# Optimization experiments

Measured on AMD Instinct MI355X. Metric: run time of the kernel, lower is better.

## Reference

```python
import jax, jax.numpy as jnp
import numpy as np
import random as pyrandom

NUM_CENTERS = 512
NUM_ITERS = 10
EPS = 1e-16
SEED = 42


def setup_inputs() -> dict:
    key = jax.random.key(0)
    x = jax.random.normal(key, (4, 16384, 256), dtype=jnp.float32)
    return {"x": x}


def _get_dist(x, v):
    # squared Euclidean distances: [B, N, K]
    x2 = jnp.sum(x * x, axis=-1, keepdims=True)            # [B, N, 1]
    xv = jnp.einsum('bnd,bkd->bnk', x, v)                  # [B, N, K]
    v2 = jnp.sum(v * v, axis=-1)[:, None, :]               # [B, 1, K]
    return jax.nn.relu(x2 - 2.0 * xv + v2)


def _update_u(x, v):
    clusters = jnp.argmin(_get_dist(x, v), axis=-1)        # [B, N]
    return jax.nn.one_hot(clusters, NUM_CENTERS, dtype=x.dtype)  # [B, N, K]


def _update_v(x, u):
    # normalize memberships over the points axis (torch dim=1 == axis -2 here)
    un = (u + EPS) / (jnp.sum(u, axis=-2, keepdims=True) + EPS)
    return jnp.einsum('bnk,bnd->bkd', un, x)               # [B, K, d]


def reference(x):
    n = x.shape[-2]
    pyrandom.seed(SEED)
    inds = np.asarray(pyrandom.sample(range(n), NUM_CENTERS))
    # initialization happens under no_grad in the original module
    v0 = jax.lax.stop_gradient(x[..., inds, :])            # [B, K, d]
    u0 = jax.lax.stop_gradient(_update_u(x, v0))

    def step(carry, _):
        _, v = carry
        u_new = _update_u(x, v)
        v_new = _update_v(x, u_new)
        return (u_new, v_new), None

    (u, v), _ = jax.lax.scan(step, (u0, v0), None, length=NUM_ITERS)
    return (u, v)
```

## Files before the change

kernel.cpp:

```cpp
#include <hip/hip_runtime.h>
#include <string.h>

#define B 4
#define N 16384
#define D 256
#define K 512
#define ITERS 10

typedef short short8 __attribute__((ext_vector_type(8)));
typedef float float4v __attribute__((ext_vector_type(4)));

static void host_sample_inds(int* out) {
    static unsigned int mt[624];
    mt[0] = 19650218u;
    for (int i = 1; i < 624; i++)
        mt[i] = 1812433253u * (mt[i - 1] ^ (mt[i - 1] >> 30)) + (unsigned)i;
    {
        int i = 1, j = 0;
        for (int kk = 624; kk; kk--) {
            mt[i] = (mt[i] ^ ((mt[i - 1] ^ (mt[i - 1] >> 30)) * 1664525u)) + 42u + (unsigned)j;
            i++; j++;
            if (i >= 624) { mt[0] = mt[623]; i = 1; }
            if (j >= 1) j = 0;
        }
        for (int kk = 623; kk; kk--) {
            mt[i] = (mt[i] ^ ((mt[i - 1] ^ (mt[i - 1] >> 30)) * 1566083941u)) - (unsigned)i;
            i++;
            if (i >= 624) { mt[0] = mt[623]; i = 1; }
        }
        mt[0] = 0x80000000u;
    }
    static unsigned char seen[N];
    memset(seen, 0, sizeof(seen));
    int mti = 624;
    int got = 0;
    while (got < K) {
        if (mti >= 624) {
            for (int kk = 0; kk < 624; kk++) {
                unsigned int yy = (mt[kk] & 0x80000000u) | (mt[(kk + 1) % 624] & 0x7fffffffu);
                mt[kk] = mt[(kk + 397) % 624] ^ (yy >> 1) ^ ((yy & 1u) ? 0x9908b0dfu : 0u);
            }
            mti = 0;
        }
        unsigned int y = mt[mti++];
        y ^= y >> 11; y ^= (y << 7) & 0x9d2c5680u; y ^= (y << 15) & 0xefc60000u; y ^= y >> 18;
        unsigned int r = y >> 17;
        if (r >= (unsigned)N) continue;
        if (seen[r]) continue;
        seen[r] = 1;
        out[got++] = (int)r;
    }
}

__device__ inline void gload_lds16(const void* g, void* l) {
    __builtin_amdgcn_global_load_lds((const __attribute__((address_space(1))) void*)g,
                                     (__attribute__((address_space(3))) void*)l, 16, 0, 0);
}

__device__ inline unsigned bf16_rne(float f) {
    unsigned u = __float_as_uint(f);
    return (u + 0x7fffu + ((u >> 16) & 1u)) >> 16;
}

__device__ inline unsigned long long shfl_xor_u64(unsigned long long v, int off) {
    int lo = __shfl_xor((int)(unsigned)(v & 0xffffffffull), off);
    int hi = __shfl_xor((int)(unsigned)(v >> 32), off);
    return ((unsigned long long)(unsigned)hi << 32) | (unsigned)lo;
}


__global__ void k_gather_v0(const float* __restrict__ x, const int* __restrict__ inds,
                            float* __restrict__ v) {
    int bk = blockIdx.x; int b = bk / K, k = bk % K;
    int n = inds[k];
    const float4* src = (const float4*)(x + ((size_t)b * N + n) * D);
    float4* dst = (float4*)(v + ((size_t)b * K + k) * D);
    dst[threadIdx.x] = src[threadIdx.x];
}

__global__ void k_totsum(const float* __restrict__ x, float* __restrict__ totsum) {
    int b = blockIdx.y;
    int n0 = blockIdx.x * (N / 64);
    int t = threadIdx.x;
    const float* xb = x + (size_t)b * N * D;
    float s = 0.f;
    for (int n = n0; n < n0 + N / 64; n++) s += xb[(size_t)n * D + t];
    atomicAdd(&totsum[b * D + t], s);
}

__global__ void k_prep(const float* __restrict__ src, unsigned short* __restrict__ cat,
                       float* __restrict__ sq, float* __restrict__ resn,
                       float* __restrict__ lon) {
    int wave = threadIdx.x >> 6, lane = threadIdx.x & 63;
    int row = blockIdx.x * 4 + wave;
    float4 f = ((const float4*)(src + (size_t)row * D))[lane];
    float comp[4] = {f.x, f.y, f.z, f.w};
    unsigned short h[4], l[4];
    float r2 = 0.f, l2 = 0.f, n2 = 0.f;
    #pragma unroll
    for (int j = 0; j < 4; j++) {
        n2 += comp[j] * comp[j];
        unsigned hi = bf16_rne(comp[j]);
        float hif = __uint_as_float(hi << 16);
        float r = comp[j] - hif;
        unsigned lo = bf16_rne(r);
        float lof = __uint_as_float(lo << 16);
        float res = r - lof;
        r2 += res * res;
        l2 += lof * lof;
        h[j] = (unsigned short)hi; l[j] = (unsigned short)lo;
    }
    unsigned short* orow = cat + (size_t)row * 512;
    *(ushort4*)&orow[lane * 4] = make_ushort4(h[0], h[1], h[2], h[3]);
    *(ushort4*)&orow[256 + lane * 4] = make_ushort4(l[0], l[1], l[2], l[3]);
    #pragma unroll
    for (int off = 32; off; off >>= 1) {
        r2 += __shfl_xor(r2, off);
        l2 += __shfl_xor(l2, off);
        n2 += __shfl_xor(n2, off);
    }
    if (lane == 0) { sq[row] = n2; resn[row] = sqrtf(r2); lon[row] = sqrtf(l2); }
}

__global__ void k_errmax(const float* __restrict__ v2, const float* __restrict__ vres,
                         const float* __restrict__ vlo,
                         float* __restrict__ vmaxs, float* __restrict__ vresmaxs,
                         float* __restrict__ vlomaxs) {
    __shared__ float s1[256], s2[256], s3[256];
    int b = blockIdx.x, t = threadIdx.x;
    s1[t] = fmaxf(sqrtf(v2[b * K + t]), sqrtf(v2[b * K + 256 + t]));
    s2[t] = fmaxf(vres[b * K + t], vres[b * K + 256 + t]);
    s3[t] = fmaxf(vlo[b * K + t], vlo[b * K + 256 + t]);
    __syncthreads();
    for (int s = 128; s; s >>= 1) {
        if (t < s) {
            s1[t] = fmaxf(s1[t], s1[t + s]);
            s2[t] = fmaxf(s2[t], s2[t + s]);
            s3[t] = fmaxf(s3[t], s3[t + s]);
        }
        __syncthreads();
    }
    if (t == 0) { vmaxs[b] = s1[0]; vresmaxs[b] = s2[0]; vlomaxs[b] = s3[0]; }
}

__global__ void k_transpose(const float* __restrict__ v, float* __restrict__ vT) {
    int idx = blockIdx.x * 256 + threadIdx.x;
    int d = idx & 255, c = (idx >> 8) & 511, b = idx >> 17;
    vT[((size_t)b * D + d) * K + c] = v[idx];
}

__global__ __launch_bounds__(256, 2) void k_gemm_assign(
    const unsigned short* __restrict__ xcat, const unsigned short* __restrict__ vcat,
    const float* __restrict__ x2, const float* __restrict__ v2,
    const float* __restrict__ xres, const float* __restrict__ xlo,
    const float* __restrict__ vmaxs, const float* __restrict__ vresmaxs,
    const float* __restrict__ vlomaxs,
    int* __restrict__ assign, int* __restrict__ counts,
    int* __restrict__ refine_cnt, int* __restrict__ refine_pt) {
    __shared__ __align__(16) unsigned short As[2][128 * 64];
    __shared__ __align__(16) unsigned short Bs[2][128 * 64];
    __shared__ float x2s[128];
    __shared__ float v2s[512];
    __shared__ unsigned long long candk[128][2][2];
    int b = blockIdx.y;
    int n0 = blockIdx.x * 128;
    int tid = threadIdx.x;
    int wv = tid >> 6, lane = tid & 63;
    int wr = wv >> 1, wc = wv & 1;
    int quad = lane >> 4, l16 = lane & 15;
    const unsigned short* xb = xcat + ((size_t)b * N + n0) * 512;
    const unsigned short* vb0 = vcat + (size_t)b * K * 512;

    if (tid < 128) x2s[tid] = x2[b * N + n0 + tid];
    v2s[tid] = v2[b * K + tid];
    v2s[tid + 256] = v2[b * K + 256 + tid];

    int lds8[4], srow[4], schunk[4];
    #pragma unroll
    for (int i = 0; i < 4; i++) {
        int l = i * 256 + wv * 64 + lane;
        lds8[i] = l * 8;
        srow[i] = l >> 3;
        schunk[i] = ((l & 7) ^ ((l >> 3) & 7)) * 8;
    }

    float4v acc[4][4];
    #pragma unroll
    for (int i = 0; i < 4; i++)
        #pragma unroll
        for (int j = 0; j < 4; j++) acc[i][j] = (float4v){0.f, 0.f, 0.f, 0.f};

    unsigned long long k1[16], k2[16];
    #pragma unroll
    for (int i = 0; i < 16; i++) { k1[i] = ~0ull; k2[i] = ~0ull; }

    #pragma unroll
    for (int i = 0; i < 4; i++) {
        gload_lds16(xb + (size_t)srow[i] * 512 + schunk[i], (void*)&As[0][lds8[i]]);
        gload_lds16(vb0 + (size_t)srow[i] * 512 + schunk[i], (void*)&Bs[0][lds8[i]]);
    }
    __syncthreads();

    for (int ch = 0; ch < 4; ch++) {
        for (int kt = 0; kt < 12; kt++) {
            int cur = kt & 1;
            int nkt = kt + 1, nch = ch;
            if (nkt == 12) { nkt = 0; nch++; }
            if (nch < 4) {
                int k4 = (nkt & 3) * 64;
                int kcolA = (nkt < 8) ? k4 : 256 + k4;
                int kcolB = (nkt < 4) ? k4 : ((nkt < 8) ? 256 + k4 : k4);
                const unsigned short* vbn = vb0 + (size_t)nch * (128 * 512);
                #pragma unroll
                for (int i = 0; i < 4; i++) {
                    gload_lds16(xb + (size_t)srow[i] * 512 + kcolA + schunk[i],
                                (void*)&As[1 - cur][lds8[i]]);
                    gload_lds16(vbn + (size_t)srow[i] * 512 + kcolB + schunk[i],
                                (void*)&Bs[1 - cur][lds8[i]]);
                }
            }
            #pragma unroll
            for (int ks = 0; ks < 2; ks++) {
                short8 af[4], bf[4];
                int ccr = ks * 4 + quad;
                #pragma unroll
                for (int f = 0; f < 4; f++) {
                    int rA = wr * 64 + f * 16 + l16;
                    af[f] = *(const short8*)&As[cur][(rA * 8 + (ccr ^ (rA & 7))) * 8];
                    int rB = wc * 64 + f * 16 + l16;
                    bf[f] = *(const short8*)&Bs[cur][(rB * 8 + (ccr ^ (rB & 7))) * 8];
                }
                #pragma unroll
                for (int fi = 0; fi < 4; fi++)
                    #pragma unroll
                    for (int fj = 0; fj < 4; fj++)
                        acc[fi][fj] = __builtin_amdgcn_mfma_f32_16x16x32_bf16(
                            af[fi], bf[fj], acc[fi][fj], 0, 0, 0);
            }
            __syncthreads();
        }
        #pragma unroll
        for (int fi = 0; fi < 4; fi++) {
            #pragma unroll
            for (int r = 0; r < 4; r++) {
                int lrow = wr * 64 + fi * 16 + quad * 4 + r;
                float x2v = x2s[lrow];
                int idx = fi * 4 + r;
                #pragma unroll
                for (int fj = 0; fj < 4; fj++) {
                    int cg = ch * 128 + wc * 64 + fj * 16 + l16;
                    float dist = fmaxf((x2v - 2.0f * acc[fi][fj][r]) + v2s[cg], 0.0f);
                    unsigned long long key =
                        ((unsigned long long)__float_as_uint(dist) << 32) | (unsigned)cg;
                    if (key < k1[idx]) { k2[idx] = k1[idx]; k1[idx] = key; }
                    else if (key < k2[idx]) { k2[idx] = key; }
                }
            }
        }
        #pragma unroll
        for (int fi = 0; fi < 4; fi++)
            #pragma unroll
            for (int fj = 0; fj < 4; fj++) acc[fi][fj] = (float4v){0.f, 0.f, 0.f, 0.f};
    }

    #pragma unroll
    for (int fi = 0; fi < 4; fi++) {
        #pragma unroll
        for (int r = 0; r < 4; r++) {
            int lrow = wr * 64 + fi * 16 + quad * 4 + r;
            int idx = fi * 4 + r;
            unsigned long long a1 = k1[idx], a2 = k2[idx];
            #pragma unroll
            for (int off = 1; off < 16; off <<= 1) {
                unsigned long long o1 = shfl_xor_u64(a1, off);
                unsigned long long o2 = shfl_xor_u64(a2, off);
                unsigned long long mx = a1 > o1 ? a1 : o1;
                a1 = a1 < o1 ? a1 : o1;
                unsigned long long mn2 = a2 < o2 ? a2 : o2;
                a2 = mx < mn2 ? mx : mn2;
            }
            if (l16 == 0) { candk[lrow][wc][0] = a1; candk[lrow][wc][1] = a2; }
        }
    }
    __syncthreads();
    if (tid < 128) {
        unsigned long long a1 = candk[tid][0][0], a2 = candk[tid][0][1];
        unsigned long long o1 = candk[tid][1][0], o2 = candk[tid][1][1];
        unsigned long long mx = a1 > o1 ? a1 : o1;
        unsigned long long b1 = a1 < o1 ? a1 : o1;
        unsigned long long mn2 = a2 < o2 ? a2 : o2;
        unsigned long long b2 = mx < mn2 ? mx : mn2;
        float bv1 = __uint_as_float((unsigned)(b1 >> 32));
        float bv2 = __uint_as_float((unsigned)(b2 >> 32));
        int bi1 = (int)(unsigned)(b1 & 0xffffffffull);
        int p = b * N + n0 + tid;
        assign[p] = bi1;
        atomicAdd(&counts[b * K + bi1], 1);
        float thr = 4.0f * (xres[p] * vmaxs[b] + sqrtf(x2s[tid]) * vresmaxs[b]
                            + xlo[p] * vlomaxs[b]) + 4e-3f;
        if (bv2 - bv1 < thr) {
            int pos = atomicAdd(refine_cnt, 1);
            refine_pt[pos] = p;
        }
    }
}

__global__ __launch_bounds__(256) void k_rescan(
    const float* __restrict__ x, const float* __restrict__ vT,
    const float* __restrict__ x2, const float* __restrict__ v2,
    const int* __restrict__ refine_cnt, const int* __restrict__ refine_pt,
    int* __restrict__ assign, int* __restrict__ counts) {
    __shared__ float xs[256];
    __shared__ float rv[256];
    __shared__ int ri[256];
    int cnt = *refine_cnt;
    int t = threadIdx.x;
    for (int i = blockIdx.x; i < cnt; i += gridDim.x) {
        int p = refine_pt[i];
        int b = p >> 14;
        xs[t] = x[(size_t)p * D + t];
        __syncthreads();
        const float* vtb = vT + (size_t)b * D * K;
        float s0 = 0.f, s1 = 0.f;
        for (int d = 0; d < D; d++) {
            float xd = xs[d];
            s0 = fmaf(xd, vtb[(size_t)d * K + t], s0);
            s1 = fmaf(xd, vtb[(size_t)d * K + 256 + t], s1);
        }
        float x2p = x2[p];
        float d0 = fmaxf((x2p - 2.0f * s0) + v2[b * K + t], 0.0f);
        float d1 = fmaxf((x2p - 2.0f * s1) + v2[b * K + 256 + t], 0.0f);
        float bv; int bi;
        if (d1 < d0) { bv = d1; bi = t + 256; } else { bv = d0; bi = t; }
        rv[t] = bv; ri[t] = bi;
        __syncthreads();
        for (int s = 128; s; s >>= 1) {
            if (t < s) {
                if (rv[t + s] < rv[t] || (rv[t + s] == rv[t] && ri[t + s] < ri[t])) {
                    rv[t] = rv[t + s]; ri[t] = ri[t + s];
                }
            }
            __syncthreads();
        }
        if (t == 0) {
            int old = assign[p];
            int neu = ri[0];
            if (neu != old) {
                assign[p] = neu;
                atomicSub(&counts[b * K + old], 1);
                atomicAdd(&counts[b * K + neu], 1);
            }
        }
        __syncthreads();
    }
}


__global__ __launch_bounds__(256) void k_scatter(
    const int* __restrict__ assign, const int* __restrict__ counts,
    int* __restrict__ cursor, int* __restrict__ order) {
    __shared__ int offs[K];
    int b = blockIdx.y;
    if (threadIdx.x < 64) {
        int lane = threadIdx.x;
        int pre[8]; int s = 0;
        #pragma unroll
        for (int j = 0; j < 8; j++) { pre[j] = s; s += counts[b * K + lane * 8 + j]; }
        int inc = s;
        #pragma unroll
        for (int off = 1; off < 64; off <<= 1) {
            int o = __shfl_up(inc, off);
            if (lane >= off) inc += o;
        }
        int excl = inc - s;
        #pragma unroll
        for (int j = 0; j < 8; j++) offs[lane * 8 + j] = excl + pre[j];
    }
    __syncthreads();
    int n = blockIdx.x * 256 + threadIdx.x;
    int a = assign[b * N + n];
    int pos = atomicAdd(&cursor[b * K + a], 1);
    order[b * N + offs[a] + pos] = n;
}

__global__ __launch_bounds__(256) void k_sumdiv(
    const float* __restrict__ x, const int* __restrict__ counts,
    const int* __restrict__ order, const float* __restrict__ totsum,
    float* __restrict__ v) {
    __shared__ int sh[256];
    __shared__ int ord[256];
    int t = threadIdx.x;
    int b = blockIdx.y, k = blockIdx.x;
    const int* cb = counts + b * K;
    int partial = 0;
    for (int j = t; j < k; j += 256) partial += cb[j];
    sh[t] = partial; __syncthreads();
    for (int s = 128; s; s >>= 1) { if (t < s) sh[t] += sh[t + s]; __syncthreads(); }
    int off = sh[0];
    int cnt = cb[k];
    const float* xb = x + (size_t)b * N * D;
    float acc = 0.f;
    for (int m0 = 0; m0 < cnt; m0 += 256) {
        int mm = min(256, cnt - m0);
        if (t < mm) ord[t] = order[b * N + off + m0 + t];
        __syncthreads();
        for (int m = 0; m < mm; m++) {
            int n = ord[m];
            acc += xb[(size_t)n * D + t];
        }
        __syncthreads();
    }
    float out;
    if (cnt > 0) out = acc * (1.0f / (float)cnt);
    else out = totsum[b * D + t];
    v[((size_t)b * K + k) * D + t] = out;
}

__global__ void k_write_u(const int* __restrict__ assign, float* __restrict__ uout) {
    int idx = blockIdx.x * 256 + threadIdx.x;
    int a = assign[idx];
    uout[(size_t)idx * K + a] = 1.0f;
}

__global__ void k_copy_v(const float* __restrict__ v, float* __restrict__ out) {
    int idx = blockIdx.x * 256 + threadIdx.x;
    ((float4*)out)[idx] = ((const float4*)v)[idx];
}

extern "C" void kernel_launch(void* const* d_in, const int* in_sizes, int n_in,
                              void* d_out, int out_size, void* d_ws, size_t ws_size,
                              hipStream_t stream) {
    const float* x = (const float*)d_in[0];
    float* out = (float*)d_out;
    char* ws = (char*)d_ws;

    size_t off = 0;
    float* v      = (float*)(ws + off); off += (size_t)B * K * D * 4;
    float* x2     = (float*)(ws + off); off += (size_t)B * N * 4;
    float* v2     = (float*)(ws + off); off += (size_t)B * K * 4;
    float* totsum = (float*)(ws + off); off += (size_t)B * D * 4;
    int* assign   = (int*)(ws + off);   off += (size_t)B * N * 4;
    int* counts   = (int*)(ws + off);   off += (size_t)B * K * 4;
    int* cursor   = (int*)(ws + off);   off += (size_t)B * K * 4;
    int* order    = (int*)(ws + off);   off += (size_t)B * N * 4;
    int* inds     = (int*)(ws + off);   off += 4096;
    int* refine_cnt = (int*)(ws + off); off += 256;

    char* ob = (char*)out;
    size_t oboff = 0;
    unsigned short* xcat = (unsigned short*)(ob + oboff); oboff += (size_t)B * N * 512 * 2;
    int* refine_pt = (int*)(ob + oboff);    oboff += (size_t)B * N * 4;
    float* vT      = (float*)(ob + oboff);  oboff += (size_t)B * K * D * 4;
    float* xres    = (float*)(ob + oboff);  oboff += (size_t)B * N * 4;
    float* xlo     = (float*)(ob + oboff);  oboff += (size_t)B * N * 4;
    float* vres    = (float*)(ob + oboff);  oboff += (size_t)B * K * 4;
    float* vlo     = (float*)(ob + oboff);  oboff += (size_t)B * K * 4;
    float* vmaxs   = (float*)(ob + oboff);  oboff += 256;
    float* vresmaxs = (float*)(ob + oboff); oboff += 256;
    float* vlomaxs = (float*)(ob + oboff);  oboff += 256;
    unsigned short* vcat = (unsigned short*)(out + (size_t)B * N * K);

    static int h_inds[K];
    host_sample_inds(h_inds);
    hipMemcpyAsync(inds, h_inds, K * sizeof(int), hipMemcpyHostToDevice, stream);

    hipMemsetAsync(totsum, 0, (size_t)B * D * 4, stream);
    k_gather_v0<<<B * K, 64, 0, stream>>>(x, inds, v);
    k_totsum<<<dim3(64, B), 256, 0, stream>>>(x, totsum);
    k_prep<<<(B * N) / 4, 256, 0, stream>>>(x, xcat, x2, xres, xlo);

    for (int it = 0; it < ITERS; it++) {
        k_prep<<<(B * K) / 4, 256, 0, stream>>>(v, vcat, v2, vres, vlo);
        k_errmax<<<B, 256, 0, stream>>>(v2, vres, vlo, vmaxs, vresmaxs, vlomaxs);
        k_transpose<<<(B * K * D) / 256, 256, 0, stream>>>(v, vT);
        hipMemsetAsync(refine_cnt, 0, 256, stream);
        hipMemsetAsync(counts, 0, 2 * (size_t)B * K * 4, stream);
        k_gemm_assign<<<dim3(N / 128, B), 256, 0, stream>>>(
            xcat, vcat, x2, v2, xres, xlo, vmaxs, vresmaxs, vlomaxs,
            assign, counts, refine_cnt, refine_pt);
        k_rescan<<<1024, 256, 0, stream>>>(x, vT, x2, v2, refine_cnt, refine_pt,
                                           assign, counts);
        k_scatter<<<dim3(N / 256, B), 256, 0, stream>>>(assign, counts, cursor, order);
        k_sumdiv<<<dim3(K, B), 256, 0, stream>>>(x, counts, order, totsum, v);
    }

    hipMemsetAsync(out, 0, (size_t)B * N * K * 4, stream);
    k_write_u<<<(B * N) / 256, 256, 0, stream>>>(assign, out);
    k_copy_v<<<(B * K * D) / 1024, 256, 0, stream>>>(v, out + (size_t)B * N * K);
}
```

Baseline: 1.625 ms.

## Replace double-buffered GEMM tiles with 4-slot half-step LDS ring and vmcnt waits

Restructures the assign GEMM main loop from a double buffer of 64-wide K tiles to a four-slot ring of 32-wide half-steps, prefetching three stages ahead. Completion is tracked with explicit vmcnt waits and raw s_barrier instead of __syncthreads each step, and MFMA priority is raised with s_setprio. The aim is deeper overlap of global-to-LDS loads with MFMA work and less barrier stall. The cost is more barriers per K-step and fragile hand-counted vmcnt values tied to the number of loads each stage issues.

```diff
diff --git a/kernel.cpp b/kernel.cpp
--- a/kernel.cpp
+++ b/kernel.cpp
@@ -157,8 +157,8 @@
     const float* __restrict__ vlomaxs,
     int* __restrict__ assign, int* __restrict__ counts,
     int* __restrict__ refine_cnt, int* __restrict__ refine_pt) {
-    __shared__ __align__(16) unsigned short As[2][128 * 64];
-    __shared__ __align__(16) unsigned short Bs[2][128 * 64];
+    __shared__ __align__(16) unsigned short ringA[4][128 * 32];
+    __shared__ __align__(16) unsigned short ringB[4][128 * 32];
     __shared__ float x2s[128];
     __shared__ float v2s[512];
     __shared__ unsigned long long candk[128][2][2];
@@ -175,13 +175,13 @@
     v2s[tid] = v2[b * K + tid];
     v2s[tid + 256] = v2[b * K + 256 + tid];
 
-    int lds8[4], srow[4], schunk[4];
+    int ldsoff[2], srow2[2], schunk2[2];
     #pragma unroll
-    for (int i = 0; i < 4; i++) {
-        int l = i * 256 + wv * 64 + lane;
-        lds8[i] = l * 8;
-        srow[i] = l >> 3;
-        schunk[i] = ((l & 7) ^ ((l >> 3) & 7)) * 8;
+    for (int i = 0; i < 2; i++) {
+        int l = i * 256 + tid;
+        ldsoff[i] = l * 8;
+        srow2[i] = l >> 2;
+        schunk2[i] = ((l & 3) ^ ((l >> 2) & 3)) * 8;
     }
 
     float4v acc[4][4];
@@ -194,51 +194,45 @@
     #pragma unroll
     for (int i = 0; i < 16; i++) { k1[i] = ~0ull; k2[i] = ~0ull; }
 
-    #pragma unroll
-    for (int i = 0; i < 4; i++) {
-        gload_lds16(xb + (size_t)srow[i] * 512 + schunk[i], (void*)&As[0][lds8[i]]);
-        gload_lds16(vb0 + (size_t)srow[i] * 512 + schunk[i], (void*)&Bs[0][lds8[i]]);
-    }
-    __syncthreads();
-
-    for (int ch = 0; ch < 4; ch++) {
-        for (int kt = 0; kt < 12; kt++) {
-            int cur = kt & 1;
-            int nkt = kt + 1, nch = ch;
-            if (nkt == 12) { nkt = 0; nch++; }
-            if (nch < 4) {
-                int k4 = (nkt & 3) * 64;
-                int kcolA = (nkt < 8) ? k4 : 256 + k4;
-                int kcolB = (nkt < 4) ? k4 : ((nkt < 8) ? 256 + k4 : k4);
-                const unsigned short* vbn = vb0 + (size_t)nch * (128 * 512);
-                #pragma unroll
-                for (int i = 0; i < 4; i++) {
-                    gload_lds16(xb + (size_t)srow[i] * 512 + kcolA + schunk[i],
-                                (void*)&As[1 - cur][lds8[i]]);
-                    gload_lds16(vbn + (size_t)srow[i] * 512 + kcolB + schunk[i],
-                                (void*)&Bs[1 - cur][lds8[i]]);
-                }
-            }
+    auto stage_hs = [&](int hs2) {
+        int ch2 = hs2 / 24;
+        int j2 = hs2 - ch2 * 24;
+        int kkt = j2 >> 1, ks = j2 & 1;
+        int k4 = ((kkt & 3) << 6) | (ks << 5);
+        int kcolA = (kkt < 8) ? k4 : 256 + k4;
+        int kcolB = (kkt < 4) ? k4 : ((kkt < 8) ? 256 + k4 : k4);
+        const unsigned short* vbn = vb0 + ((size_t)ch2 << 16);
+        unsigned short* dA = &ringA[0][0] + ((hs2 & 3) << 12);
+        unsigned short* dB = &ringB[0][0] + ((hs2 & 3) << 12);
+        #pragma unroll
+        for (int i = 0; i < 2; i++) {
+            gload_lds16(xb + (size_t)srow2[i] * 512 + kcolA + schunk2[i], dA + ldsoff[i]);
+            gload_lds16(vbn + (size_t)srow2[i] * 512 + kcolB + schunk2[i], dB + ldsoff[i]);
+        }
+    };
+
+    auto compute_hs = [&](int slot) {
+        const unsigned short* As_ = &ringA[0][0] + (slot << 12);
+        const unsigned short* Bs_ = &ringB[0][0] + (slot << 12);
+        short8 af[4], bf[4];
+        #pragma unroll
+        for (int f = 0; f < 4; f++) {
+            int rA = wr * 64 + f * 16 + l16;
+            af[f] = *(const short8*)&As_[(rA * 4 + (quad ^ (rA & 3))) * 8];
+            int rB = wc * 64 + f * 16 + l16;
+            bf[f] = *(const short8*)&Bs_[(rB * 4 + (quad ^ (rB & 3))) * 8];
+        }
+        __builtin_amdgcn_s_setprio(1);
+        #pragma unroll
+        for (int fi = 0; fi < 4; fi++)
             #pragma unroll
-            for (int ks = 0; ks < 2; ks++) {
-                short8 af[4], bf[4];
-                int ccr = ks * 4 + quad;
-                #pragma unroll
-                for (int f = 0; f < 4; f++) {
-                    int rA = wr * 64 + f * 16 + l16;
-                    af[f] = *(const short8*)&As[cur][(rA * 8 + (ccr ^ (rA & 7))) * 8];
-                    int rB = wc * 64 + f * 16 + l16;
-                    bf[f] = *(const short8*)&Bs[cur][(rB * 8 + (ccr ^ (rB & 7))) * 8];
-                }
-                #pragma unroll
-                for (int fi = 0; fi < 4; fi++)
-                    #pragma unroll
-                    for (int fj = 0; fj < 4; fj++)
-                        acc[fi][fj] = __builtin_amdgcn_mfma_f32_16x16x32_bf16(
-                            af[fi], bf[fj], acc[fi][fj], 0, 0, 0);
-            }
-            __syncthreads();
-        }
+            for (int fj = 0; fj < 4; fj++)
+                acc[fi][fj] = __builtin_amdgcn_mfma_f32_16x16x32_bf16(
+                    af[fi], bf[fj], acc[fi][fj], 0, 0, 0);
+        __builtin_amdgcn_s_setprio(0);
+    };
+
+    auto fold = [&](int ch) {
         #pragma unroll
         for (int fi = 0; fi < 4; fi++) {
             #pragma unroll
@@ -261,7 +255,33 @@
         for (int fi = 0; fi < 4; fi++)
             #pragma unroll
             for (int fj = 0; fj < 4; fj++) acc[fi][fj] = (float4v){0.f, 0.f, 0.f, 0.f};
-    }
+    };
+
+    stage_hs(0); stage_hs(1); stage_hs(2);
+    asm volatile("s_waitcnt lgkmcnt(0)" ::: "memory");
+    __builtin_amdgcn_s_barrier();
+
+    for (int hs = 0; hs < 93; hs++) {
+        asm volatile("s_waitcnt vmcnt(8)" ::: "memory");
+        __builtin_amdgcn_s_barrier();
+        __builtin_amdgcn_sched_barrier(0);
+        stage_hs(hs + 3);
+        compute_hs(hs & 3);
+        if ((hs % 24) == 23) fold(hs / 24);
+    }
+    asm volatile("s_waitcnt vmcnt(8)" ::: "memory");
+    __builtin_amdgcn_s_barrier();
+    __builtin_amdgcn_sched_barrier(0);
+    compute_hs(93 & 3);
+    asm volatile("s_waitcnt vmcnt(4)" ::: "memory");
+    __builtin_amdgcn_s_barrier();
+    __builtin_amdgcn_sched_barrier(0);
+    compute_hs(94 & 3);
+    asm volatile("s_waitcnt vmcnt(0)" ::: "memory");
+    __builtin_amdgcn_s_barrier();
+    __builtin_amdgcn_sched_barrier(0);
+    compute_hs(95 & 3);
+    fold(3);
 
     #pragma unroll
     for (int fi = 0; fi < 4; fi++) {
```

New measurement: 1.832 ms. 1.13x slower.
